# Optimization experiments

Measured on AMD Instinct MI355X. Metric: run time of the kernel, lower is better.

Reference implementation:

```python
import jax, jax.numpy as jnp
import numpy as np

N = 50000      # nodes
E = 800000     # edges
D = 96         # in_dim = out_dim
ED = 17        # edge_dim = RBF_BINS + 1


def setup_inputs() -> dict:
    key = jax.random.key(0)
    ks = jax.random.split(key, 12)
    x = jax.random.normal(ks[0], (N, D), dtype=jnp.float32)
    edge_index = jax.random.randint(ks[1], (2, E), 0, N, dtype=jnp.int64)
    edge_attr = jax.random.uniform(ks[2], (E, ED), dtype=jnp.float32)
    s = 1.0 / np.sqrt(ED)
    W1 = jax.random.uniform(ks[3], (D, ED), jnp.float32, -s, s)
    b1 = jax.random.uniform(ks[4], (D,), jnp.float32, -s, s)
    s = 1.0 / np.sqrt(D)
    W2 = jax.random.uniform(ks[5], (D, D), jnp.float32, -s, s)
    b2 = jax.random.uniform(ks[6], (D,), jnp.float32, -s, s)
    Ws = jax.random.uniform(ks[7], (D, D), jnp.float32, -s, s)
    bs = jax.random.uniform(ks[8], (D,), jnp.float32, -s, s)
    Wn = jax.random.uniform(ks[9], (D, D), jnp.float32, -s, s)
    bn = jax.random.uniform(ks[10], (D,), jnp.float32, -s, s)
    return {"x": x, "edge_index": edge_index, "edge_attr": edge_attr,
            "W1": W1, "b1": b1, "W2": W2, "b2": b2,
            "Ws": Ws, "bs": bs, "Wn": Wn, "bn": bn}


def reference(x, edge_index, edge_attr, W1, b1, W2, b2, Ws, bs, Wn, bn):
    src, dst = edge_index[0], edge_index[1]
    # edge MLP: Linear -> ReLU -> Linear  => per-edge weight [E, D]
    h = jax.nn.relu(edge_attr @ W1.T + b1)
    w = h @ W2.T + b2
    # gather node features at src, weight, scatter-add into dst
    msg = w * x[src]                                   # [E, D]
    agg = jax.ops.segment_sum(msg, dst, num_segments=x.shape[0])  # [N, D]
    return jax.nn.relu(x @ Ws.T + bs + agg @ Wn.T + bn)
```

## Files before the change

### kernel.cpp

```cpp
#include <hip/hip_runtime.h>

#define BLOCK 512
#define TE 64
#define TN 64
#define NTB 512

typedef float f32x4 __attribute__((ext_vector_type(4)));
typedef short s16x8 __attribute__((ext_vector_type(8)));

static __device__ __forceinline__ unsigned short f2bf(float f) {
    unsigned int u = __float_as_uint(f);
    u += 0x7FFFu + ((u >> 16) & 1u);
    return (unsigned short)(u >> 16);
}
static __device__ __forceinline__ float bf2f(unsigned short s) {
    return __uint_as_float(((unsigned int)s) << 16);
}

__global__ __launch_bounds__(BLOCK, 4) void edge_kernel(
    const float* __restrict__ x,
    const int*   __restrict__ ei,
    const float* __restrict__ ea,
    const float* __restrict__ W1,
    const float* __restrict__ b1,
    const float* __restrict__ W2,
    const float* __restrict__ b2,
    float* __restrict__ agg,
    int N, int E)
{
    __shared__ unsigned short sBh[9216];
    __shared__ unsigned short sBl[9216];
    __shared__ unsigned short sAh[3][TE][40];
    __shared__ unsigned short sAl[3][TE][40];
    __shared__ float sW1[96][20];
    __shared__ float sea[TE][20];
    __shared__ float sb1[96];
    __shared__ int   ssrc[TE], sdst[TE];

    const int tid  = threadIdx.x;
    const int c    = tid & 31;
    const int g    = tid >> 5;
    const int lane = tid & 63;
    const int wv   = tid >> 6;
    const int mr   = wv & 3;
    const int ng   = wv >> 2;
    const int l15  = lane & 15;
    const int l4   = lane >> 4;

    const int ntiles = (E + TE - 1) / TE;

    const int pe = tid >> 3, ps = tid & 7;
    float pf0 = 0.f, pf1 = 0.f, pf2 = 0.f; int pidx = 0;
    int tile = blockIdx.x;
    {
        int e0n = tile * TE;
        int ee  = e0n + pe; if (ee >= E) ee = E - 1;
        const float* er = ea + (size_t)ee * 17;
        pf0 = er[ps];
        pf1 = er[ps + 8];
        if (ps == 0) pf2 = er[16];
        if (tid < TE)            { int e = e0n + tid;      pidx = (e < E) ? ei[e]     : 0; }
        else if (tid < 2 * TE)   { int e = e0n + tid - TE; pidx = (e < E) ? ei[E + e] : 0; }
    }

    for (int idx = tid; idx < 96 * 20; idx += BLOCK) {
        int d = idx / 20, k = idx - d * 20;
        sW1[d][k] = (k < 17) ? W1[d * 17 + k] : 0.f;
    }
    for (int idx = tid; idx < 96 * 96; idx += BLOCK) {
        int d = idx / 96, k = idx - d * 96;
        float v = W2[idx];
        unsigned short hb = f2bf(v);
        int ngf = d / 48, tt = (d % 48) / 16, r = d & 15;
        int ch = k >> 5, kl4 = (k & 31) >> 3, sb = k & 7;
        int fo = ((((ngf * 3 + tt) * 3 + ch) * 4 + kl4) * 16 + r) * 8 + sb;
        sBh[fo] = hb;
        sBl[fo] = f2bf(v - bf2f(hb));
    }
    if (tid < 96) sb1[tid] = b1[tid];
    if (tid < TE) { sea[tid][17] = 0.f; sea[tid][18] = 0.f; sea[tid][19] = 0.f; }

    float bias[3]; int dv[3];
    #pragma unroll
    for (int t = 0; t < 3; ++t) {
        dv[t]   = (ng * 3 + t) * 16 + l15;
        bias[t] = b2[dv[t]];
    }

    __syncthreads();

    sea[pe][ps]     = pf0;
    sea[pe][ps + 8] = pf1;
    if (ps == 0) sea[pe][16] = pf2;
    if (tid < TE)          ssrc[tid]      = pidx;
    else if (tid < 2 * TE) sdst[tid - TE] = pidx;
    __syncthreads();

    float p_wvx[12]; int p_dn[4]; int p_e0 = 0;
    const int first = blockIdx.x;

    for (; tile < ntiles; tile += NTB) {
        const int nxt = tile + NTB;

        if (tile != first) {
            #pragma unroll
            for (int t = 0; t < 3; ++t)
                #pragma unroll
                for (int j = 0; j < 4; ++j) {
                    int e = p_e0 + mr * 16 + l4 * 4 + j;
                    if (e < E)
                        atomicAdd(&agg[(size_t)p_dn[j] * 96 + dv[t]], p_wvx[t * 4 + j]);
                }
        }

        if (nxt < ntiles) {
            int e0n = nxt * TE;
            int ee  = e0n + pe; if (ee >= E) ee = E - 1;
            const float* er = ea + (size_t)ee * 17;
            pf0 = er[ps];
            pf1 = er[ps + 8];
            if (ps == 0) pf2 = er[16];
            if (tid < TE)            { int e = e0n + tid;      pidx = (e < E) ? ei[e]     : 0; }
            else if (tid < 2 * TE)   { int e = e0n + tid - TE; pidx = (e < E) ? ei[E + e] : 0; }
        }

        int sg[4], ndn[4];
        #pragma unroll
        for (int j = 0; j < 4; ++j) {
            int elj = mr * 16 + l4 * 4 + j;
            sg[j]  = ssrc[elj];
            ndn[j] = sdst[elj];
        }
        float xg[12];
        #pragma unroll
        for (int t = 0; t < 3; ++t)
            #pragma unroll
            for (int j = 0; j < 4; ++j)
                xg[t * 4 + j] = x[(size_t)sg[j] * 96 + dv[t]];

        {
            float hacc[4][3];
            #pragma unroll
            for (int i = 0; i < 4; ++i) {
                hacc[i][0] = sb1[c]; hacc[i][1] = sb1[c + 32]; hacc[i][2] = sb1[c + 64];
            }
            #pragma unroll
            for (int k0 = 0; k0 < 20; k0 += 4) {
                float4 w0 = *(const float4*)&sW1[c][k0];
                float4 w1 = *(const float4*)&sW1[c + 32][k0];
                float4 w2 = *(const float4*)&sW1[c + 64][k0];
                #pragma unroll
                for (int i = 0; i < 4; ++i) {
                    float4 av = *(const float4*)&sea[g * 4 + i][k0];
                    hacc[i][0] = fmaf(av.w, w0.w, fmaf(av.z, w0.z, fmaf(av.y, w0.y, fmaf(av.x, w0.x, hacc[i][0]))));
                    hacc[i][1] = fmaf(av.w, w1.w, fmaf(av.z, w1.z, fmaf(av.y, w1.y, fmaf(av.x, w1.x, hacc[i][1]))));
                    hacc[i][2] = fmaf(av.w, w2.w, fmaf(av.z, w2.z, fmaf(av.y, w2.y, fmaf(av.x, w2.x, hacc[i][2]))));
                }
            }
            #pragma unroll
            for (int i = 0; i < 4; ++i) {
                int e = g * 4 + i;
                #pragma unroll
                for (int j = 0; j < 3; ++j) {
                    float v = fmaxf(hacc[i][j], 0.f);
                    unsigned short hb = f2bf(v);
                    sAh[j][e][c] = hb;
                    sAl[j][e][c] = f2bf(v - bf2f(hb));
                }
            }
        }
        __syncthreads();

        f32x4 acc[3];
        #pragma unroll
        for (int t = 0; t < 3; ++t) acc[t] = (f32x4){0.f, 0.f, 0.f, 0.f};
        const int arow = mr * 16 + l15;
        #pragma unroll
        for (int chunk = 0; chunk < 3; ++chunk) {
            s16x8 a_hi = *(const s16x8*)&sAh[chunk][arow][l4 * 8];
            s16x8 a_lo = *(const s16x8*)&sAl[chunk][arow][l4 * 8];
            #pragma unroll
            for (int t = 0; t < 3; ++t) {
                const int base = (((ng * 3 + t) * 3 + chunk) * 64 + lane) * 8;
                s16x8 b_hi = *(const s16x8*)&sBh[base];
                s16x8 b_lo = *(const s16x8*)&sBl[base];
                acc[t] = __builtin_amdgcn_mfma_f32_16x16x32_bf16(a_hi, b_hi, acc[t], 0, 0, 0);
                acc[t] = __builtin_amdgcn_mfma_f32_16x16x32_bf16(a_hi, b_lo, acc[t], 0, 0, 0);
                acc[t] = __builtin_amdgcn_mfma_f32_16x16x32_bf16(a_lo, b_hi, acc[t], 0, 0, 0);
            }
        }

        if (nxt < ntiles) {
            sea[pe][ps]     = pf0;
            sea[pe][ps + 8] = pf1;
            if (ps == 0) sea[pe][16] = pf2;
            if (tid < TE)          ssrc[tid]      = pidx;
            else if (tid < 2 * TE) sdst[tid - TE] = pidx;
        }

        #pragma unroll
        for (int t = 0; t < 3; ++t)
            #pragma unroll
            for (int j = 0; j < 4; ++j)
                p_wvx[t * 4 + j] = (acc[t][j] + bias[t]) * xg[t * 4 + j];
        #pragma unroll
        for (int j = 0; j < 4; ++j) p_dn[j] = ndn[j];
        p_e0 = tile * TE;

        __syncthreads();
    }

    if (first < ntiles) {
        #pragma unroll
        for (int t = 0; t < 3; ++t)
            #pragma unroll
            for (int j = 0; j < 4; ++j) {
                int e = p_e0 + mr * 16 + l4 * 4 + j;
                if (e < E)
                    atomicAdd(&agg[(size_t)p_dn[j] * 96 + dv[t]], p_wvx[t * 4 + j]);
            }
    }
}

__global__ __launch_bounds__(BLOCK, 4) void node_kernel(
    const float* __restrict__ x,
    const float* __restrict__ agg,
    const float* __restrict__ Ws, const float* __restrict__ bs,
    const float* __restrict__ Wn, const float* __restrict__ bn,
    float* __restrict__ out, int N)
{
    __shared__ float sW[96][100];
    __shared__ float sxa[TN][100];
    __shared__ float sbias[96];

    const int tid = threadIdx.x;
    const int c = tid & 31, g = tid >> 5;
    const int n0 = blockIdx.x * TN;

    if (tid < 96) sbias[tid] = bs[tid] + bn[tid];

    float acc[4][3];
    #pragma unroll
    for (int i = 0; i < 4; ++i)
        for (int j = 0; j < 3; ++j) acc[i][j] = 0.f;

    for (int ph = 0; ph < 2; ++ph) {
        const float* __restrict__ W   = ph ? Wn : Ws;
        const float* __restrict__ src = ph ? agg : x;
        __syncthreads();
        for (int idx = tid; idx < 96 * 24; idx += BLOCK) {
            int d = idx / 24, kq = idx - d * 24;
            *(float4*)&sW[d][kq * 4] = *(const float4*)&W[d * 96 + kq * 4];
        }
        for (int idx = tid; idx < TN * 24; idx += BLOCK) {
            int n = idx / 24, kq = idx - n * 24;
            float4 v = make_float4(0.f, 0.f, 0.f, 0.f);
            if (n0 + n < N) v = *(const float4*)&src[(size_t)(n0 + n) * 96 + kq * 4];
            *(float4*)&sxa[n][kq * 4] = v;
        }
        __syncthreads();
        #pragma unroll 2
        for (int k0 = 0; k0 < 96; k0 += 4) {
            float4 w0 = *(const float4*)&sW[c][k0];
            float4 w1 = *(const float4*)&sW[c + 32][k0];
            float4 w2 = *(const float4*)&sW[c + 64][k0];
            #pragma unroll
            for (int i = 0; i < 4; ++i) {
                float4 xv = *(const float4*)&sxa[g * 4 + i][k0];
                acc[i][0] = fmaf(xv.w, w0.w, fmaf(xv.z, w0.z, fmaf(xv.y, w0.y, fmaf(xv.x, w0.x, acc[i][0]))));
                acc[i][1] = fmaf(xv.w, w1.w, fmaf(xv.z, w1.z, fmaf(xv.y, w1.y, fmaf(xv.x, w1.x, acc[i][1]))));
                acc[i][2] = fmaf(xv.w, w2.w, fmaf(xv.z, w2.z, fmaf(xv.y, w2.y, fmaf(xv.x, w2.x, acc[i][2]))));
            }
        }
    }

    #pragma unroll
    for (int i = 0; i < 4; ++i) {
        int n = n0 + g * 4 + i;
        if (n < N) {
            out[(size_t)n * 96 + c]      = fmaxf(acc[i][0] + sbias[c], 0.f);
            out[(size_t)n * 96 + c + 32] = fmaxf(acc[i][1] + sbias[c + 32], 0.f);
            out[(size_t)n * 96 + c + 64] = fmaxf(acc[i][2] + sbias[c + 64], 0.f);
        }
    }
}

extern "C" void kernel_launch(void* const* d_in, const int* in_sizes, int n_in,
                              void* d_out, int out_size, void* d_ws, size_t ws_size,
                              hipStream_t stream) {
    const float* x  = (const float*)d_in[0];
    const int*   ei = (const int*)d_in[1];
    const float* ea = (const float*)d_in[2];
    const float* W1 = (const float*)d_in[3];
    const float* b1 = (const float*)d_in[4];
    const float* W2 = (const float*)d_in[5];
    const float* b2 = (const float*)d_in[6];
    const float* Ws = (const float*)d_in[7];
    const float* bs = (const float*)d_in[8];
    const float* Wn = (const float*)d_in[9];
    const float* bn = (const float*)d_in[10];
    float* out = (float*)d_out;

    const int N = in_sizes[0] / 96;
    const int E = in_sizes[2] / 17;

    float* agg = (ws_size >= (size_t)N * 96 * sizeof(float)) ? (float*)d_ws : out;
    hipMemsetAsync(agg, 0, (size_t)N * 96 * sizeof(float), stream);

    edge_kernel<<<NTB, BLOCK, 0, stream>>>(x, ei, ea, W1, b1, W2, b2, agg, N, E);
    node_kernel<<<(N + TN - 1) / TN, BLOCK, 0, stream>>>(x, agg, Ws, bs, Wn, bn, out, N);
}
```

Measured before the change: 319.4 us.

## Sort edges by destination into CSR and accumulate messages in shared memory

```diff
diff --git a/kernel.cpp b/kernel.cpp
--- a/kernel.cpp
+++ b/kernel.cpp
@@ -1,9 +1,10 @@
 #include <hip/hip_runtime.h>
 
-#define BLOCK 512
-#define TE 64
+#define NPB 98
+#define TEK 128
+#define EBLK 1024
+#define NBLK 512
 #define TN 64
-#define NTB 512
 
 typedef float f32x4 __attribute__((ext_vector_type(4)));
 typedef short s16x8 __attribute__((ext_vector_type(8)));
@@ -17,57 +18,101 @@
     return __uint_as_float(((unsigned int)s) << 16);
 }
 
-__global__ __launch_bounds__(BLOCK, 4) void edge_kernel(
+static __device__ __forceinline__ void bar_sync() {
+    __builtin_amdgcn_sched_barrier(0);
+    asm volatile("s_waitcnt lgkmcnt(0)");
+    __builtin_amdgcn_s_barrier();
+    __builtin_amdgcn_sched_barrier(0);
+}
+
+__global__ void hist_kernel(const int* __restrict__ ei, int* __restrict__ cnt, int E) {
+    int e = blockIdx.x * blockDim.x + threadIdx.x;
+    if (e < E) atomicAdd(&cnt[ei[E + e]], 1);
+}
+
+__global__ __launch_bounds__(1024) void scan_kernel(int* __restrict__ cur,
+                                                    int* __restrict__ rs, int N, int E) {
+    __shared__ int s[1024];
+    const int tid = threadIdx.x;
+    const int chunk = (N + 1023) >> 10;
+    const int base = tid * chunk;
+    const int end  = min(base + chunk, N);
+    int local = 0;
+    for (int i = base; i < end; ++i) local += cur[i];
+    s[tid] = local;
+    __syncthreads();
+    for (int off = 1; off < 1024; off <<= 1) {
+        int v = (tid >= off) ? s[tid - off] : 0;
+        __syncthreads();
+        s[tid] += v;
+        __syncthreads();
+    }
+    int run = s[tid] - local;
+    for (int i = base; i < end; ++i) {
+        int c = cur[i];
+        rs[i]  = run;
+        cur[i] = run;
+        run += c;
+    }
+    if (tid == 0) rs[N] = E;
+}
+
+__global__ void scatter_kernel(const int* __restrict__ ei, int* __restrict__ cur,
+                               int* __restrict__ meta, int* __restrict__ srcs, int E) {
+    int e = blockIdx.x * blockDim.x + threadIdx.x;
+    if (e < E) {
+        int d   = ei[E + e];
+        int pos = atomicAdd(&cur[d], 1);
+        meta[pos] = ((d % NPB) << 20) | e;
+        srcs[pos] = ei[e];
+    }
+}
+
+__global__ __launch_bounds__(EBLK, 4) void edge_csr_kernel(
     const float* __restrict__ x,
-    const int*   __restrict__ ei,
     const float* __restrict__ ea,
     const float* __restrict__ W1,
     const float* __restrict__ b1,
     const float* __restrict__ W2,
     const float* __restrict__ b2,
-    float* __restrict__ agg,
+    const int*   __restrict__ rs,
+    const int*   __restrict__ meta,
+    const int*   __restrict__ srcs,
+    float* agg,
     int N, int E)
 {
-    __shared__ unsigned short sBh[9216];
-    __shared__ unsigned short sBl[9216];
-    __shared__ unsigned short sAh[3][TE][40];
-    __shared__ unsigned short sAl[3][TE][40];
+    __shared__ unsigned short sBh[9216], sBl[9216];
+    __shared__ unsigned short sAh[3][TEK][40];
+    __shared__ unsigned short sAl[3][TEK][40];
     __shared__ float sW1[96][20];
-    __shared__ float sea[TE][20];
+    __shared__ float sea[TEK][20];
+    __shared__ float accum[NPB][96];
     __shared__ float sb1[96];
-    __shared__ int   ssrc[TE], sdst[TE];
+    __shared__ int   s_src[TEK], s_dloc[TEK];
 
     const int tid  = threadIdx.x;
     const int c    = tid & 31;
-    const int g    = tid >> 5;
+    const int g    = (tid >> 5) & 15;
+    const int sub  = tid >> 9;
+    const int es0  = sub * 64;
     const int lane = tid & 63;
-    const int wv   = tid >> 6;
-    const int mr   = wv & 3;
-    const int ng   = wv >> 2;
+    const int wv8  = (tid >> 6) & 7;
+    const int mr   = wv8 & 3;
+    const int ng   = wv8 >> 2;
     const int l15  = lane & 15;
     const int l4   = lane >> 4;
 
-    const int ntiles = (E + TE - 1) / TE;
-
-    const int pe = tid >> 3, ps = tid & 7;
-    float pf0 = 0.f, pf1 = 0.f, pf2 = 0.f; int pidx = 0;
-    int tile = blockIdx.x;
-    {
-        int e0n = tile * TE;
-        int ee  = e0n + pe; if (ee >= E) ee = E - 1;
-        const float* er = ea + (size_t)ee * 17;
-        pf0 = er[ps];
-        pf1 = er[ps + 8];
-        if (ps == 0) pf2 = er[16];
-        if (tid < TE)            { int e = e0n + tid;      pidx = (e < E) ? ei[e]     : 0; }
-        else if (tid < 2 * TE)   { int e = e0n + tid - TE; pidx = (e < E) ? ei[E + e] : 0; }
-    }
-
-    for (int idx = tid; idx < 96 * 20; idx += BLOCK) {
+    const int nb0    = blockIdx.x * NPB;
+    const int ebeg   = rs[min(nb0, N)];
+    const int eend   = rs[min(nb0 + NPB, N)];
+    const int ecount = eend - ebeg;
+    const int ntiles = (ecount + TEK - 1) / TEK;
+
+    for (int idx = tid; idx < 96 * 20; idx += EBLK) {
         int d = idx / 20, k = idx - d * 20;
         sW1[d][k] = (k < 17) ? W1[d * 17 + k] : 0.f;
     }
-    for (int idx = tid; idx < 96 * 96; idx += BLOCK) {
+    for (int idx = tid; idx < 96 * 96; idx += EBLK) {
         int d = idx / 96, k = idx - d * 96;
         float v = W2[idx];
         unsigned short hb = f2bf(v);
@@ -78,7 +123,8 @@
         sBl[fo] = f2bf(v - bf2f(hb));
     }
     if (tid < 96) sb1[tid] = b1[tid];
-    if (tid < TE) { sea[tid][17] = 0.f; sea[tid][18] = 0.f; sea[tid][19] = 0.f; }
+    if (tid < TEK) { sea[tid][17] = 0.f; sea[tid][18] = 0.f; sea[tid][19] = 0.f; }
+    for (int idx = tid; idx < NPB * 96; idx += EBLK) (&accum[0][0])[idx] = 0.f;
 
     float bias[3]; int dv[3];
     #pragma unroll
@@ -87,56 +133,62 @@
         bias[t] = b2[dv[t]];
     }
 
+    const int pe = tid >> 3, ps = tid & 7;
+    float pf0 = 0.f, pf1 = 0.f, pf2 = 0.f;
+    int sp_src = 0, sp_meta = 0;
+    if (ntiles > 0) {
+        int gi = min(ebeg + pe, E - 1);
+        int m  = meta[gi];
+        const float* er = ea + (size_t)(m & 0xFFFFF) * 17;
+        pf0 = er[ps];
+        pf1 = er[ps + 8];
+        if (ps == 0) pf2 = er[16];
+        if (tid < TEK) {
+            int gj = min(ebeg + tid, E - 1);
+            sp_meta = meta[gj];
+            sp_src  = srcs[gj];
+        }
+    }
     __syncthreads();
-
-    sea[pe][ps]     = pf0;
-    sea[pe][ps + 8] = pf1;
-    if (ps == 0) sea[pe][16] = pf2;
-    if (tid < TE)          ssrc[tid]      = pidx;
-    else if (tid < 2 * TE) sdst[tid - TE] = pidx;
+    if (ntiles > 0) {
+        sea[pe][ps]     = pf0;
+        sea[pe][ps + 8] = pf1;
+        if (ps == 0) sea[pe][16] = pf2;
+        if (tid < TEK) { s_src[tid] = sp_src; s_dloc[tid] = sp_meta >> 20; }
+    }
     __syncthreads();
 
-    float p_wvx[12]; int p_dn[4]; int p_e0 = 0;
-    const int first = blockIdx.x;
-
-    for (; tile < ntiles; tile += NTB) {
-        const int nxt = tile + NTB;
-
-        if (tile != first) {
-            #pragma unroll
-            for (int t = 0; t < 3; ++t)
-                #pragma unroll
-                for (int j = 0; j < 4; ++j) {
-                    int e = p_e0 + mr * 16 + l4 * 4 + j;
-                    if (e < E)
-                        atomicAdd(&agg[(size_t)p_dn[j] * 96 + dv[t]], p_wvx[t * 4 + j]);
-                }
-        }
-
-        if (nxt < ntiles) {
-            int e0n = nxt * TE;
-            int ee  = e0n + pe; if (ee >= E) ee = E - 1;
-            const float* er = ea + (size_t)ee * 17;
+    for (int t = 0; t < ntiles; ++t) {
+        const bool nxt = (t + 1) < ntiles;
+        const int  rem = ecount - t * TEK;
+
+        int sg[4], dl[4];
+        #pragma unroll
+        for (int j = 0; j < 4; ++j) {
+            int el = es0 + mr * 16 + l4 * 4 + j;
+            sg[j] = s_src[el];
+            dl[j] = s_dloc[el];
+        }
+        float xg[12];
+        #pragma unroll
+        for (int tt = 0; tt < 3; ++tt)
+            #pragma unroll
+            for (int j = 0; j < 4; ++j)
+                xg[tt * 4 + j] = x[(size_t)sg[j] * 96 + dv[tt]];
+
+        if (nxt) {
+            int gi = min(ebeg + (t + 1) * TEK + pe, E - 1);
+            int m  = meta[gi];
+            const float* er = ea + (size_t)(m & 0xFFFFF) * 17;
             pf0 = er[ps];
             pf1 = er[ps + 8];
             if (ps == 0) pf2 = er[16];
-            if (tid < TE)            { int e = e0n + tid;      pidx = (e < E) ? ei[e]     : 0; }
-            else if (tid < 2 * TE)   { int e = e0n + tid - TE; pidx = (e < E) ? ei[E + e] : 0; }
-        }
-
-        int sg[4], ndn[4];
-        #pragma unroll
-        for (int j = 0; j < 4; ++j) {
-            int elj = mr * 16 + l4 * 4 + j;
-            sg[j]  = ssrc[elj];
-            ndn[j] = sdst[elj];
-        }
-        float xg[12];
-        #pragma unroll
-        for (int t = 0; t < 3; ++t)
-            #pragma unroll
-            for (int j = 0; j < 4; ++j)
-                xg[t * 4 + j] = x[(size_t)sg[j] * 96 + dv[t]];
+            if (tid < TEK) {
+                int gj = min(ebeg + (t + 1) * TEK + tid, E - 1);
+                sp_meta = meta[gj];
+                sp_src  = srcs[gj];
+            }
+        }
 
         {
             float hacc[4][3];
@@ -144,6 +196,135 @@
             for (int i = 0; i < 4; ++i) {
                 hacc[i][0] = sb1[c]; hacc[i][1] = sb1[c + 32]; hacc[i][2] = sb1[c + 64];
             }
+            #pragma unroll
+            for (int k0 = 0; k0 < 20; k0 += 4) {
+                float4 w0 = *(const float4*)&sW1[c][k0];
+                float4 w1 = *(const float4*)&sW1[c + 32][k0];
+                float4 w2 = *(const float4*)&sW1[c + 64][k0];
+                #pragma unroll
+                for (int i = 0; i < 4; ++i) {
+                    float4 av = *(const float4*)&sea[es0 + g * 4 + i][k0];
+                    hacc[i][0] = fmaf(av.w, w0.w, fmaf(av.z, w0.z, fmaf(av.y, w0.y, fmaf(av.x, w0.x, hacc[i][0]))));
+                    hacc[i][1] = fmaf(av.w, w1.w, fmaf(av.z, w1.z, fmaf(av.y, w1.y, fmaf(av.x, w1.x, hacc[i][1]))));
+                    hacc[i][2] = fmaf(av.w, w2.w, fmaf(av.z, w2.z, fmaf(av.y, w2.y, fmaf(av.x, w2.x, hacc[i][2]))));
+                }
+            }
+            #pragma unroll
+            for (int i = 0; i < 4; ++i) {
+                int e = es0 + g * 4 + i;
+                #pragma unroll
+                for (int j = 0; j < 3; ++j) {
+                    float v = fmaxf(hacc[i][j], 0.f);
+                    unsigned short hb = f2bf(v);
+                    sAh[j][e][c] = hb;
+                    sAl[j][e][c] = f2bf(v - bf2f(hb));
+                }
+            }
+        }
+        bar_sync();
+
+        f32x4 acc[3];
+        #pragma unroll
+        for (int t3 = 0; t3 < 3; ++t3) acc[t3] = (f32x4){0.f, 0.f, 0.f, 0.f};
+        const int arow = es0 + mr * 16 + l15;
+        #pragma unroll
+        for (int chunk = 0; chunk < 3; ++chunk) {
+            s16x8 a_hi = *(const s16x8*)&sAh[chunk][arow][l4 * 8];
+            s16x8 a_lo = *(const s16x8*)&sAl[chunk][arow][l4 * 8];
+            #pragma unroll
+            for (int t3 = 0; t3 < 3; ++t3) {
+                const int base = (((ng * 3 + t3) * 3 + chunk) * 64 + lane) * 8;
+                s16x8 b_hi = *(const s16x8*)&sBh[base];
+                s16x8 b_lo = *(const s16x8*)&sBl[base];
+                acc[t3] = __builtin_amdgcn_mfma_f32_16x16x32_bf16(a_hi, b_hi, acc[t3], 0, 0, 0);
+                acc[t3] = __builtin_amdgcn_mfma_f32_16x16x32_bf16(a_hi, b_lo, acc[t3], 0, 0, 0);
+                acc[t3] = __builtin_amdgcn_mfma_f32_16x16x32_bf16(a_lo, b_hi, acc[t3], 0, 0, 0);
+            }
+        }
+
+        if (nxt) {
+            sea[pe][ps]     = pf0;
+            sea[pe][ps + 8] = pf1;
+            if (ps == 0) sea[pe][16] = pf2;
+            if (tid < TEK) { s_src[tid] = sp_src; s_dloc[tid] = sp_meta >> 20; }
+        }
+
+        #pragma unroll
+        for (int t3 = 0; t3 < 3; ++t3)
+            #pragma unroll
+            for (int j = 0; j < 4; ++j) {
+                int el = es0 + mr * 16 + l4 * 4 + j;
+                if (el < rem)
+                    atomicAdd(&accum[dl[j]][dv[t3]], (acc[t3][j] + bias[t3]) * xg[t3 * 4 + j]);
+            }
+
+        bar_sync();
+    }
+
+    __syncthreads();
+    for (int idx = tid; idx < NPB * 96; idx += EBLK) {
+        int n = nb0 + idx / 96;
+        if (n < N) agg[(size_t)n * 96 + (idx % 96)] = (&accum[0][0])[idx];
+    }
+}
+
+__global__ __launch_bounds__(512, 4) void edge_kernel_atomic(
+    const float* __restrict__ x, const int* __restrict__ ei,
+    const float* __restrict__ ea, const float* __restrict__ W1,
+    const float* __restrict__ b1, const float* __restrict__ W2,
+    const float* __restrict__ b2, float* __restrict__ agg, int N, int E)
+{
+    __shared__ unsigned short sBh[9216], sBl[9216];
+    __shared__ unsigned short sAh[3][64][40], sAl[3][64][40];
+    __shared__ float sW1[96][20];
+    __shared__ float sea[64][20];
+    __shared__ float sb1[96];
+    __shared__ int   ssrc[64], sdst[64];
+
+    const int tid = threadIdx.x;
+    const int c = tid & 31, g = tid >> 5;
+    const int lane = tid & 63, wv = tid >> 6;
+    const int mr = wv & 3, ng = wv >> 2;
+    const int l15 = lane & 15, l4 = lane >> 4;
+    const int ntiles = (E + 63) / 64;
+
+    for (int idx = tid; idx < 96 * 20; idx += 512) {
+        int d = idx / 20, k = idx - d * 20;
+        sW1[d][k] = (k < 17) ? W1[d * 17 + k] : 0.f;
+    }
+    for (int idx = tid; idx < 96 * 96; idx += 512) {
+        int d = idx / 96, k = idx - d * 96;
+        float v = W2[idx];
+        unsigned short hb = f2bf(v);
+        int ngf = d / 48, tt = (d % 48) / 16, r = d & 15;
+        int ch = k >> 5, kl4 = (k & 31) >> 3, sb = k & 7;
+        int fo = ((((ngf * 3 + tt) * 3 + ch) * 4 + kl4) * 16 + r) * 8 + sb;
+        sBh[fo] = hb; sBl[fo] = f2bf(v - bf2f(hb));
+    }
+    if (tid < 96) sb1[tid] = b1[tid];
+    float bias[3]; int dv[3];
+    #pragma unroll
+    for (int t = 0; t < 3; ++t) { dv[t] = (ng * 3 + t) * 16 + l15; bias[t] = b2[dv[t]]; }
+
+    for (int tile = blockIdx.x; tile < ntiles; tile += 512) {
+        const int e0 = tile * 64;
+        __syncthreads();
+        for (int idx = tid; idx < 64 * 20; idx += 512) {
+            int e = idx / 20, k = idx - e * 20;
+            float v = 0.f;
+            if (k < 17 && e0 + e < E) v = ea[(size_t)(e0 + e) * 17 + k];
+            sea[e][k] = v;
+        }
+        if (tid < 64) {
+            int e = e0 + tid;
+            ssrc[tid] = (e < E) ? ei[e] : 0;
+            sdst[tid] = (e < E) ? ei[E + e] : 0;
+        }
+        __syncthreads();
+        {
+            float hacc[4][3];
+            #pragma unroll
+            for (int i = 0; i < 4; ++i) { hacc[i][0]=sb1[c]; hacc[i][1]=sb1[c+32]; hacc[i][2]=sb1[c+64]; }
             #pragma unroll
             for (int k0 = 0; k0 < 20; k0 += 4) {
                 float4 w0 = *(const float4*)&sW1[c][k0];
@@ -164,13 +345,11 @@
                 for (int j = 0; j < 3; ++j) {
                     float v = fmaxf(hacc[i][j], 0.f);
                     unsigned short hb = f2bf(v);
-                    sAh[j][e][c] = hb;
-                    sAl[j][e][c] = f2bf(v - bf2f(hb));
+                    sAh[j][e][c] = hb; sAl[j][e][c] = f2bf(v - bf2f(hb));
                 }
             }
         }
         __syncthreads();
-
         f32x4 acc[3];
         #pragma unroll
         for (int t = 0; t < 3; ++t) acc[t] = (f32x4){0.f, 0.f, 0.f, 0.f};
@@ -189,45 +368,27 @@
                 acc[t] = __builtin_amdgcn_mfma_f32_16x16x32_bf16(a_lo, b_hi, acc[t], 0, 0, 0);
             }
         }
-
-        if (nxt < ntiles) {
-            sea[pe][ps]     = pf0;
-            sea[pe][ps + 8] = pf1;
-            if (ps == 0) sea[pe][16] = pf2;
-            if (tid < TE)          ssrc[tid]      = pidx;
-            else if (tid < 2 * TE) sdst[tid - TE] = pidx;
-        }
-
         #pragma unroll
         for (int t = 0; t < 3; ++t)
             #pragma unroll
-            for (int j = 0; j < 4; ++j)
-                p_wvx[t * 4 + j] = (acc[t][j] + bias[t]) * xg[t * 4 + j];
-        #pragma unroll
-        for (int j = 0; j < 4; ++j) p_dn[j] = ndn[j];
-        p_e0 = tile * TE;
-
-        __syncthreads();
-    }
-
-    if (first < ntiles) {
-        #pragma unroll
-        for (int t = 0; t < 3; ++t)
-            #pragma unroll
             for (int j = 0; j < 4; ++j) {
-                int e = p_e0 + mr * 16 + l4 * 4 + j;
-                if (e < E)
-                    atomicAdd(&agg[(size_t)p_dn[j] * 96 + dv[t]], p_wvx[t * 4 + j]);
-            }
-    }
-}
-
-__global__ __launch_bounds__(BLOCK, 4) void node_kernel(
+                int el = mr * 16 + l4 * 4 + j;
+                int e  = e0 + el;
+                if (e < E) {
+                    int s = ssrc[el], dn = sdst[el];
+                    atomicAdd(&agg[(size_t)dn * 96 + dv[t]],
+                              (acc[t][j] + bias[t]) * x[(size_t)s * 96 + dv[t]]);
+                }
+            }
+    }
+}
+
+__global__ __launch_bounds__(NBLK, 4) void node_kernel(
     const float* __restrict__ x,
-    const float* __restrict__ agg,
+    const float* agg,
     const float* __restrict__ Ws, const float* __restrict__ bs,
     const float* __restrict__ Wn, const float* __restrict__ bn,
-    float* __restrict__ out, int N)
+    float* out, int N)
 {
     __shared__ float sW[96][100];
     __shared__ float sxa[TN][100];
@@ -245,14 +406,14 @@
         for (int j = 0; j < 3; ++j) acc[i][j] = 0.f;
 
     for (int ph = 0; ph < 2; ++ph) {
-        const float* __restrict__ W   = ph ? Wn : Ws;
-        const float* __restrict__ src = ph ? agg : x;
-        __syncthreads();
-        for (int idx = tid; idx < 96 * 24; idx += BLOCK) {
+        const float* W   = ph ? Wn : Ws;
+        const float* src = ph ? agg : x;
+        __syncthreads();
+        for (int idx = tid; idx < 96 * 24; idx += NBLK) {
             int d = idx / 24, kq = idx - d * 24;
             *(float4*)&sW[d][kq * 4] = *(const float4*)&W[d * 96 + kq * 4];
         }
-        for (int idx = tid; idx < TN * 24; idx += BLOCK) {
+        for (int idx = tid; idx < TN * 24; idx += NBLK) {
             int n = idx / 24, kq = idx - n * 24;
             float4 v = make_float4(0.f, 0.f, 0.f, 0.f);
             if (n0 + n < N) v = *(const float4*)&src[(size_t)(n0 + n) * 96 + kq * 4];
@@ -304,9 +465,23 @@
     const int N = in_sizes[0] / 96;
     const int E = in_sizes[2] / 17;
 
-    float* agg = (ws_size >= (size_t)N * 96 * sizeof(float)) ? (float*)d_ws : out;
-    hipMemsetAsync(agg, 0, (size_t)N * 96 * sizeof(float), stream);
-
-    edge_kernel<<<NTB, BLOCK, 0, stream>>>(x, ei, ea, W1, b1, W2, b2, agg, N, E);
-    node_kernel<<<(N + TN - 1) / TN, BLOCK, 0, stream>>>(x, agg, Ws, bs, Wn, bn, out, N);
-}
+    const size_t need = ((size_t)2 * N + 1 + (size_t)2 * E) * sizeof(int);
+    if (ws_size >= need) {
+        int* rs   = (int*)d_ws;
+        int* cur  = rs + (N + 1);
+        int* meta = cur + N;
+        int* srcs = meta + E;
+
+        hipMemsetAsync(cur, 0, (size_t)N * sizeof(int), stream);
+        hist_kernel<<<(E + 255) / 256, 256, 0, stream>>>(ei, cur, E);
+        scan_kernel<<<1, 1024, 0, stream>>>(cur, rs, N, E);
+        scatter_kernel<<<(E + 255) / 256, 256, 0, stream>>>(ei, cur, meta, srcs, E);
+        edge_csr_kernel<<<(N + NPB - 1) / NPB, EBLK, 0, stream>>>(
+            x, ea, W1, b1, W2, b2, rs, meta, srcs, out, N, E);
+        node_kernel<<<(N + TN - 1) / TN, NBLK, 0, stream>>>(x, out, Ws, bs, Wn, bn, out, N);
+    } else {
+        hipMemsetAsync(out, 0, (size_t)N * 96 * sizeof(float), stream);
+        edge_kernel_atomic<<<512, 512, 0, stream>>>(x, ei, ea, W1, b1, W2, b2, out, N, E);
+        node_kernel<<<(N + TN - 1) / TN, NBLK, 0, stream>>>(x, out, Ws, bs, Wn, bn, out, N);
+    }
+}
```

New measurement: 778.6 us. 144% more time.
